# Kernel tuning notes

Hardware: AMD Instinct MI355X
Metric: run time of the kernel (lower is better)

Reference implementation:

```python
import jax, jax.numpy as jnp
import numpy as np

N_NODES = 262144
B_GRAPHS = 1024
NODES_PER_GRAPH = N_NODES // B_GRAPHS
LATENT = 256
HIDDEN = 512
OUT = 3


def setup_inputs() -> dict:
    key = jax.random.key(0)
    ks = jax.random.split(key, 8)
    feat = jax.random.normal(ks[0], (N_NODES, LATENT), dtype=jnp.float32)
    positions = jax.random.normal(ks[1], (N_NODES, 3), dtype=jnp.float32)
    cell = jax.random.normal(ks[2], (B_GRAPHS, 3, 3), dtype=jnp.float32)
    # half of graphs are non-PBC (all-zero cell) -> torque removal applied there
    cell = cell.at[: B_GRAPHS // 2].set(0.0)
    n_node = jnp.full((B_GRAPHS,), NODES_PER_GRAPH, dtype=jnp.int32)
    W0 = jax.random.normal(ks[3], (LATENT, HIDDEN), dtype=jnp.float32) / np.sqrt(LATENT)
    b0 = jnp.zeros((HIDDEN,), dtype=jnp.float32)
    W1 = jax.random.normal(ks[4], (HIDDEN, HIDDEN), dtype=jnp.float32) / np.sqrt(HIDDEN)
    b1 = jnp.zeros((HIDDEN,), dtype=jnp.float32)
    W2 = jax.random.normal(ks[5], (HIDDEN, OUT), dtype=jnp.float32) / np.sqrt(HIDDEN)
    b2 = jnp.zeros((OUT,), dtype=jnp.float32)
    return dict(feat=feat, positions=positions, cell=cell, n_node=n_node,
                W0=W0, b0=b0, W1=W1, b1=b1, W2=W2, b2=b2)


def _mlp(x, W0, b0, W1, b1, W2, b2):
    h = jax.nn.silu(x @ W0 + b0)
    h = jax.nn.silu(h @ W1 + b1)
    return h @ W2 + b2  # [N, 3], raw logits (no output activation)


def _node_head(feat, positions, cell, seg, n_node, W0, b0, W1, b1, W2, b2):
    B = n_node.shape[0]
    counts = n_node.astype(feat.dtype)[:, None]  # [B,1]
    pred = _mlp(feat, W0, b0, W1, b1, W2, b2)  # [N,3]
    # remove per-graph mean
    mean_pred = jax.ops.segment_sum(pred, seg, num_segments=B) / counts
    pred = pred - mean_pred[seg]
    # remove net torque (per-graph analytic Lagrange solution)
    com = jax.ops.segment_sum(positions, seg, num_segments=B) / counts
    r = positions - com[seg]  # com-relative positions [N,3]
    tau = jax.ops.segment_sum(jnp.cross(r, pred), seg, num_segments=B)  # [B,3]
    s = jax.ops.segment_sum(jnp.sum(r * r, axis=1), seg, num_segments=B)  # [B]
    S = jax.ops.segment_sum(r[:, :, None] * r[:, None, :], seg, num_segments=B)  # [B,3,3]
    M = S - s[:, None, None] * jnp.eye(3, dtype=feat.dtype)
    mu = jnp.linalg.solve(M, (-tau)[:, :, None])[:, :, 0]  # [B,3]
    delta = jnp.cross(r, mu[seg])  # [N,3]
    # apply torque removal only to non-PBC graphs (cell all zeros)
    nopbc = jnp.all(cell == 0.0, axis=(1, 2))  # [B]
    return jnp.where(nopbc[seg][:, None], pred + delta, pred)


def reference(feat, positions, cell, n_node, W0, b0, W1, b1, W2, b2):
    N = feat.shape[0]
    B = n_node.shape[0]
    seg = jnp.repeat(jnp.arange(B), n_node, total_repeat_length=N)
    return _node_head(feat, positions, cell, seg, n_node, W0, b0, W1, b1, W2, b2)
```

## Files before the change

### kernel.cpp

```cpp
#include <hip/hip_runtime.h>

#define N_NODES 262144
#define BGRAPHS 1024
#define NPG 256
#define LATENT 256
#define HIDDEN 512
#define BM 128

typedef unsigned short ushort_t;
typedef __attribute__((ext_vector_type(4))) float  f32x4;
typedef __attribute__((ext_vector_type(8))) short  short8;
typedef __attribute__((ext_vector_type(4))) int    int4v;
typedef __attribute__((ext_vector_type(2))) unsigned int uint2v;
typedef __attribute__((ext_vector_type(4))) float  float4v;

__device__ __forceinline__ unsigned int f2bf(float f) {
  union { float f; unsigned int u; } v; v.f = f;
  unsigned int u = v.u;
  return (u + 0x7fffu + ((u >> 16) & 1u)) >> 16;
}
__device__ __forceinline__ unsigned int cvtpk(float lo, float hi) {
  unsigned int r;
  asm("v_cvt_pk_bf16_f32 %0, %1, %2" : "=v"(r) : "v"(lo), "v"(hi));
  return r;
}
__device__ __forceinline__ float silu_f(float x) {
  return x * __builtin_amdgcn_rcpf(1.0f + __expf(-x));
}

__global__ void prep_weights(const float* __restrict__ W0, const float* __restrict__ W1,
                             ushort_t* __restrict__ W0pre, ushort_t* __restrict__ W1pre) {
  int c = blockIdx.x * 256 + threadIdx.x;
  const int C0 = 16384;
  const float* src;
  ushort_t* dst;
  int cc;
  if (c < C0) { src = W0; dst = W0pre; cc = c; }
  else        { src = W1; dst = W1pre; cc = c - C0; }
  int kstep = cc >> 11;
  int p = (cc >> 9) & 3;
  int n = cc & 511;
  int kb = kstep * 32 + p * 8;
  unsigned w[4];
#pragma unroll
  for (int j = 0; j < 4; ++j) {
    unsigned lo = f2bf(src[(size_t)(kb + 2 * j) * HIDDEN + n]);
    unsigned hi = f2bf(src[(size_t)(kb + 2 * j + 1) * HIDDEN + n]);
    w[j] = lo | (hi << 16);
  }
  *(int4v*)(dst + (size_t)cc * 8) = *(int4v*)w;
}

__global__ __launch_bounds__(512) void fused_mlp(
    const float* __restrict__ feat, const ushort_t* __restrict__ W0pre,
    const ushort_t* __restrict__ W1pre, const float* __restrict__ b0,
    const float* __restrict__ b1, const float* __restrict__ W2,
    const float* __restrict__ b2, float* __restrict__ pred) {
  __shared__ __align__(16) char Hc[131072];
  float* Pp = (float*)Hc;

  const int tid = threadIdx.x;
  const int wid = tid >> 6;
  const int lane = tid & 63;
  const int llo = lane & 15;
  const int lhi = lane >> 4;
  const int m0 = blockIdx.x * BM;

  const char* wp = (const char*)W0pre + lhi * 8192 + (wid * 64 + llo) * 16;
  short8 wf0[4], wf1[4];
#pragma unroll
  for (int nt = 0; nt < 4; ++nt) wf0[nt] = *(const short8*)(wp + nt * 256);

  {
    const int m = tid >> 2, q = tid & 3;
    const float* ap = feat + (size_t)(m0 + m) * LATENT + q * 64;
#pragma unroll
    for (int j = 0; j < 2; ++j) {
      const int cch = 2 * q + j;
#pragma unroll
      for (int p = 0; p < 4; ++p) {
        float4v x = *(const float4v*)(ap + j * 32 + p * 8);
        float4v y = *(const float4v*)(ap + j * 32 + p * 8 + 4);
        unsigned u[4];
        u[0] = cvtpk(x[0], x[1]);
        u[1] = cvtpk(x[2], x[3]);
        u[2] = cvtpk(y[0], y[1]);
        u[3] = cvtpk(y[2], y[3]);
        *(int4v*)(Hc + ((cch * 16 + p * 4 + (m >> 5)) << 10) + 512 +
                  (((m & 31) ^ (p << 3)) << 4)) = *(int4v*)u;
      }
    }
  }
  __syncthreads();

  f32x4 acc[4][8];
#pragma unroll
  for (int nt = 0; nt < 4; ++nt)
#pragma unroll
    for (int mt = 0; mt < 8; ++mt) acc[nt][mt] = 0.0f;

  const char* ab = Hc + lhi * 4096 + 512;
  const int xe = ((llo ^ (lhi << 3)) << 4);
  const int xo = (((16 + llo) ^ (lhi << 3)) << 4);

#define MFMA_ALL(WF, XF)                                                                 \
  __builtin_amdgcn_s_setprio(1);                                                         \
  _Pragma("unroll") for (int nt = 0; nt < 4; ++nt)                                       \
  _Pragma("unroll") for (int mt = 0; mt < 8; ++mt)                                       \
      acc[nt][mt] = __builtin_amdgcn_mfma_f32_16x16x32_bf16(WF[nt], XF[mt], acc[nt][mt], \
                                                            0, 0, 0);                    \
  __builtin_amdgcn_s_setprio(0);

#define G1_STEP(SOFF, WA, WB)                                                            \
  {                                                                                      \
    _Pragma("unroll") for (int nt = 0; nt < 4; ++nt)                                     \
        WB[nt] = *(const short8*)(wpp + 32768 + (SOFF) * 32768 + nt * 256);              \
    short8 xf[8];                                                                        \
    _Pragma("unroll") for (int mt = 0; mt < 8; ++mt)                                     \
        xf[mt] = *(const short8*)(abp + (SOFF) * 16384 + ((mt >> 1) << 10) +             \
                                  ((mt & 1) ? xo : xe));                                 \
    MFMA_ALL(WA, xf)                                                                     \
  }

  {
    const char* wpp = wp;
    const char* abp = ab;
#pragma unroll 1
    for (int s = 0; s < 8; s += 2) {
      G1_STEP(0, wf0, wf1)
      G1_STEP(1, wf1, wf0)
      wpp += 65536;
      abp += 32768;
    }
  }

  __syncthreads();
#pragma unroll
  for (int nt = 0; nt < 4; ++nt) {
    int nb = wid * 64 + nt * 16 + lhi * 4;
    float4v bv = *(const float4v*)(b0 + nb);
#pragma unroll
    for (int mt = 0; mt < 8; ++mt) {
      int m = mt * 16 + llo;
      float s0 = silu_f(acc[nt][mt][0] + bv[0]);
      float s1 = silu_f(acc[nt][mt][1] + bv[1]);
      float s2 = silu_f(acc[nt][mt][2] + bv[2]);
      float s3 = silu_f(acc[nt][mt][3] + bv[3]);
      uint2v pk;
      pk.x = cvtpk(s0, s1);
      pk.y = cvtpk(s2, s3);
      *(uint2v*)(Hc + m * 1024 + ((nb * 2) ^ (llo << 4))) = pk;
    }
  }
#pragma unroll
  for (int nt = 0; nt < 4; ++nt)
#pragma unroll
    for (int mt = 0; mt < 8; ++mt) acc[nt][mt] = 0.0f;
  __syncthreads();

#define G2_STEP(T, WA, WB)                                                               \
  {                                                                                      \
    if ((T) < 15) {                                                                      \
      _Pragma("unroll") for (int nt = 0; nt < 4; ++nt)                                   \
          WB[nt] = *(const short8*)(wpp + 32768 + ((T)&1) * 32768 + nt * 256);           \
    }                                                                                    \
    const int col = (((T) * 64 + lhi * 16) ^ (llo << 4));                                \
    short8 xf[8];                                                                        \
    _Pragma("unroll") for (int mt = 0; mt < 8; ++mt)                                     \
        xf[mt] = *(const short8*)(Hc + (mt * 16 + llo) * 1024 + col);                    \
    MFMA_ALL(WA, xf)                                                                     \
  }

  {
    const char* wpp = wp + 8 * 32768;
#pragma unroll 1
    for (int t = 0; t < 16; t += 2) {
      G2_STEP(t, wf0, wf1)
      G2_STEP(t + 1, wf1, wf0)
      wpp += 65536;
    }
  }

  float pacc[8][3];
#pragma unroll
  for (int mt = 0; mt < 8; ++mt) { pacc[mt][0] = 0.f; pacc[mt][1] = 0.f; pacc[mt][2] = 0.f; }
#pragma unroll
  for (int nt = 0; nt < 4; ++nt) {
    int nb = wid * 64 + nt * 16 + lhi * 4;
    float4v bv = *(const float4v*)(b1 + nb);
#pragma unroll
    for (int r = 0; r < 4; ++r) {
      float w20 = W2[(nb + r) * 3 + 0];
      float w21 = W2[(nb + r) * 3 + 1];
      float w22 = W2[(nb + r) * 3 + 2];
#pragma unroll
      for (int mt = 0; mt < 8; ++mt) {
        float h = silu_f(acc[nt][mt][r] + bv[r]);
        pacc[mt][0] += h * w20; pacc[mt][1] += h * w21; pacc[mt][2] += h * w22;
      }
    }
  }
  __syncthreads();
#pragma unroll
  for (int mt = 0; mt < 8; ++mt)
#pragma unroll
    for (int o = 0; o < 3; ++o) {
      float v = pacc[mt][o];
      v += __shfl_xor(v, 16);
      v += __shfl_xor(v, 32);
      if (lane < 16) Pp[wid * 384 + (mt * 16 + llo) * 3 + o] = v;
    }
  __syncthreads();
  if (tid < 384) {
    int m = tid / 3, o = tid - m * 3;
    float v = b2[o];
#pragma unroll
    for (int ww = 0; ww < 8; ++ww) v += Pp[ww * 384 + m * 3 + o];
    pred[(size_t)(m0 + m) * 3 + o] = v;
  }
}

template<int NV>
__device__ __forceinline__ void block_reduce(const float* v, float (*sc)[16], int wid, int lane,
                                             float* tot) {
#pragma unroll
  for (int j = 0; j < NV; ++j) {
    float x = v[j];
#pragma unroll
    for (int off = 32; off >= 1; off >>= 1) x += __shfl_down(x, off);
    if (lane == 0) sc[wid][j] = x;
  }
  __syncthreads();
#pragma unroll
  for (int j = 0; j < NV; ++j) tot[j] = sc[0][j] + sc[1][j] + sc[2][j] + sc[3][j];
  __syncthreads();
}

__global__ __launch_bounds__(256) void finalize_kernel(
    const float* __restrict__ pred, const float* __restrict__ pos,
    const float* __restrict__ cell, const int* __restrict__ n_node,
    float* __restrict__ out) {
  __shared__ float sc[4][16];
  int g = blockIdx.x, tid = threadIdx.x;
  int wid = tid >> 6, lane = tid & 63;
  size_t i = (size_t)g * NPG + tid;

  float p0 = pred[i * 3 + 0], p1 = pred[i * 3 + 1], p2 = pred[i * 3 + 2];
  float q0 = pos[i * 3 + 0], q1 = pos[i * 3 + 1], q2 = pos[i * 3 + 2];

  float v1[6] = {p0, p1, p2, q0, q1, q2};
  float t1[6];
  block_reduce<6>(v1, sc, wid, lane, t1);

  float cnt = (float)n_node[g];
  float pc0 = p0 - t1[0] / cnt, pc1 = p1 - t1[1] / cnt, pc2 = p2 - t1[2] / cnt;
  float r0 = q0 - t1[3] / cnt, r1 = q1 - t1[4] / cnt, r2 = q2 - t1[5] / cnt;

  float v2[10] = {r1 * pc2 - r2 * pc1, r2 * pc0 - r0 * pc2, r0 * pc1 - r1 * pc0,
                  r0 * r0 + r1 * r1 + r2 * r2,
                  r0 * r0, r0 * r1, r0 * r2, r1 * r1, r1 * r2, r2 * r2};
  float t2[10];
  block_reduce<10>(v2, sc, wid, lane, t2);

  double s = (double)t2[3];
  double a = (double)t2[4] - s, b = (double)t2[5], c = (double)t2[6];
  double d = (double)t2[7] - s, e = (double)t2[8], f = (double)t2[9] - s;
  double A00 = d * f - e * e;
  double A01 = c * e - b * f;
  double A02 = b * e - c * d;
  double A11 = a * f - c * c;
  double A12 = b * c - a * e;
  double A22 = a * d - b * b;
  double det = a * A00 + b * A01 + c * A02;
  double rinv = 1.0 / det;
  double rhs0 = -(double)t2[0], rhs1 = -(double)t2[1], rhs2 = -(double)t2[2];
  double mu0 = (A00 * rhs0 + A01 * rhs1 + A02 * rhs2) * rinv;
  double mu1 = (A01 * rhs0 + A11 * rhs1 + A12 * rhs2) * rinv;
  double mu2 = (A02 * rhs0 + A12 * rhs1 + A22 * rhs2) * rinv;

  bool nopbc = true;
#pragma unroll
  for (int j = 0; j < 9; ++j) nopbc = nopbc && (cell[g * 9 + j] == 0.0f);

  float d0 = (float)((double)r1 * mu2 - (double)r2 * mu1);
  float d1 = (float)((double)r2 * mu0 - (double)r0 * mu2);
  float d2 = (float)((double)r0 * mu1 - (double)r1 * mu0);

  out[i * 3 + 0] = pc0 + (nopbc ? d0 : 0.0f);
  out[i * 3 + 1] = pc1 + (nopbc ? d1 : 0.0f);
  out[i * 3 + 2] = pc2 + (nopbc ? d2 : 0.0f);
}

extern "C" void kernel_launch(void* const* d_in, const int* in_sizes, int n_in,
                              void* d_out, int out_size, void* d_ws, size_t ws_size,
                              hipStream_t stream) {
  const float* feat = (const float*)d_in[0];
  const float* positions = (const float*)d_in[1];
  const float* cell = (const float*)d_in[2];
  const int* n_node = (const int*)d_in[3];
  const float* W0 = (const float*)d_in[4];
  const float* b0 = (const float*)d_in[5];
  const float* W1 = (const float*)d_in[6];
  const float* b1 = (const float*)d_in[7];
  const float* W2 = (const float*)d_in[8];
  const float* b2 = (const float*)d_in[9];
  float* out = (float*)d_out;

  char* ws = (char*)d_ws;
  ushort_t* W0pre = (ushort_t*)ws;
  ushort_t* W1pre = (ushort_t*)(ws + 262144);
  float* pred = (float*)(ws + 786432);

  hipLaunchKernelGGL(prep_weights, dim3(192), dim3(256), 0, stream, W0, W1, W0pre, W1pre);
  hipLaunchKernelGGL(fused_mlp, dim3(N_NODES / BM), dim3(512), 0, stream,
                     feat, W0pre, W1pre, b0, b1, W2, b2, pred);
  hipLaunchKernelGGL(finalize_kernel, dim3(BGRAPHS), dim3(256), 0, stream, pred, positions, cell,
                     n_node, out);
}
```

Baseline: 248.5 us.

## Split MLP block into 16 waves with 2x8 warp tiling and fewer accumulators

The fused MLP kernel moves from 8 waves to 16 waves per block. Waves are arranged as 2 row groups by 8 column groups, so each wave holds a 64x64 accumulator tile instead of 128x64. This halves accumulator registers and drops the double-buffered weight fragments in favour of a single buffer refilled after each MFMA batch. The aim is more waves per CU for latency hiding. In exchange, weight fragments are loaded twice as often per block and the weight prefetch no longer overlaps the MFMAs as before.

Result: slower. 420.0 us (+69.0%).

```diff
diff --git a/kernel.cpp b/kernel.cpp
--- a/kernel.cpp
+++ b/kernel.cpp
@@ -51,7 +51,7 @@
   *(int4v*)(dst + (size_t)cc * 8) = *(int4v*)w;
 }
 
-__global__ __launch_bounds__(512) void fused_mlp(
+__global__ __launch_bounds__(1024, 4) void fused_mlp(
     const float* __restrict__ feat, const ushort_t* __restrict__ W0pre,
     const ushort_t* __restrict__ W1pre, const float* __restrict__ b0,
     const float* __restrict__ b1, const float* __restrict__ W2,
@@ -64,84 +64,74 @@
   const int lane = tid & 63;
   const int llo = lane & 15;
   const int lhi = lane >> 4;
+  const int wr = wid & 1;
+  const int wc = wid >> 1;
   const int m0 = blockIdx.x * BM;
 
-  const char* wp = (const char*)W0pre + lhi * 8192 + (wid * 64 + llo) * 16;
-  short8 wf0[4], wf1[4];
-#pragma unroll
-  for (int nt = 0; nt < 4; ++nt) wf0[nt] = *(const short8*)(wp + nt * 256);
+  const char* wp = (const char*)W0pre + lhi * 8192 + (wc * 64 + llo) * 16;
+  short8 wf[4];
+#pragma unroll
+  for (int nt = 0; nt < 4; ++nt) wf[nt] = *(const short8*)(wp + nt * 256);
 
   {
-    const int m = tid >> 2, q = tid & 3;
-    const float* ap = feat + (size_t)(m0 + m) * LATENT + q * 64;
-#pragma unroll
-    for (int j = 0; j < 2; ++j) {
-      const int cch = 2 * q + j;
-#pragma unroll
-      for (int p = 0; p < 4; ++p) {
-        float4v x = *(const float4v*)(ap + j * 32 + p * 8);
-        float4v y = *(const float4v*)(ap + j * 32 + p * 8 + 4);
-        unsigned u[4];
-        u[0] = cvtpk(x[0], x[1]);
-        u[1] = cvtpk(x[2], x[3]);
-        u[2] = cvtpk(y[0], y[1]);
-        u[3] = cvtpk(y[2], y[3]);
-        *(int4v*)(Hc + ((cch * 16 + p * 4 + (m >> 5)) << 10) + 512 +
-                  (((m & 31) ^ (p << 3)) << 4)) = *(int4v*)u;
-      }
-    }
-  }
-  __syncthreads();
-
-  f32x4 acc[4][8];
+    const int m = tid >> 3, cch = tid & 7;
+    const float* ap = feat + (size_t)(m0 + m) * LATENT + cch * 32;
+#pragma unroll
+    for (int p = 0; p < 4; ++p) {
+      float4v x = *(const float4v*)(ap + p * 8);
+      float4v y = *(const float4v*)(ap + p * 8 + 4);
+      unsigned u[4];
+      u[0] = cvtpk(x[0], x[1]);
+      u[1] = cvtpk(x[2], x[3]);
+      u[2] = cvtpk(y[0], y[1]);
+      u[3] = cvtpk(y[2], y[3]);
+      *(int4v*)(Hc + ((cch * 16 + p * 4 + (m >> 5)) << 10) + 512 +
+                (((m & 31) ^ (p << 3)) << 4)) = *(int4v*)u;
+    }
+  }
+  __syncthreads();
+
+  f32x4 acc[4][4];
 #pragma unroll
   for (int nt = 0; nt < 4; ++nt)
 #pragma unroll
-    for (int mt = 0; mt < 8; ++mt) acc[nt][mt] = 0.0f;
-
-  const char* ab = Hc + lhi * 4096 + 512;
-  const int xe = ((llo ^ (lhi << 3)) << 4);
-  const int xo = (((16 + llo) ^ (lhi << 3)) << 4);
-
-#define MFMA_ALL(WF, XF)                                                                 \
+    for (int mt = 0; mt < 4; ++mt) acc[nt][mt] = 0.0f;
+
+#define MFMA_ALL(XF)                                                                     \
   __builtin_amdgcn_s_setprio(1);                                                         \
   _Pragma("unroll") for (int nt = 0; nt < 4; ++nt)                                       \
-  _Pragma("unroll") for (int mt = 0; mt < 8; ++mt)                                       \
-      acc[nt][mt] = __builtin_amdgcn_mfma_f32_16x16x32_bf16(WF[nt], XF[mt], acc[nt][mt], \
+  _Pragma("unroll") for (int mt = 0; mt < 4; ++mt)                                       \
+      acc[nt][mt] = __builtin_amdgcn_mfma_f32_16x16x32_bf16(wf[nt], XF[mt], acc[nt][mt], \
                                                             0, 0, 0);                    \
   __builtin_amdgcn_s_setprio(0);
 
-#define G1_STEP(SOFF, WA, WB)                                                            \
-  {                                                                                      \
-    _Pragma("unroll") for (int nt = 0; nt < 4; ++nt)                                     \
-        WB[nt] = *(const short8*)(wpp + 32768 + (SOFF) * 32768 + nt * 256);              \
-    short8 xf[8];                                                                        \
-    _Pragma("unroll") for (int mt = 0; mt < 8; ++mt)                                     \
-        xf[mt] = *(const short8*)(abp + (SOFF) * 16384 + ((mt >> 1) << 10) +             \
-                                  ((mt & 1) ? xo : xe));                                 \
-    MFMA_ALL(WA, xf)                                                                     \
-  }
-
   {
+    const char* abp = Hc + 512 + (lhi * 4 + wr * 2) * 1024;
+    const int xe = ((llo ^ (lhi << 3)) << 4);
+    const int xo = (((16 + llo) ^ (lhi << 3)) << 4);
     const char* wpp = wp;
-    const char* abp = ab;
 #pragma unroll 1
-    for (int s = 0; s < 8; s += 2) {
-      G1_STEP(0, wf0, wf1)
-      G1_STEP(1, wf1, wf0)
-      wpp += 65536;
-      abp += 32768;
+    for (int s = 0; s < 8; ++s) {
+      short8 xf[4];
+#pragma unroll
+      for (int mt = 0; mt < 4; ++mt)
+        xf[mt] = *(const short8*)(abp + ((mt >> 1) << 10) + ((mt & 1) ? xo : xe));
+      MFMA_ALL(xf)
+#pragma unroll
+      for (int nt = 0; nt < 4; ++nt) wf[nt] = *(const short8*)(wpp + 32768 + nt * 256);
+      wpp += 32768;
+      abp += 16384;
     }
   }
 
   __syncthreads();
 #pragma unroll
   for (int nt = 0; nt < 4; ++nt) {
-    int nb = wid * 64 + nt * 16 + lhi * 4;
+    int nb = wc * 64 + nt * 16 + lhi * 4;
     float4v bv = *(const float4v*)(b0 + nb);
 #pragma unroll
-    for (int mt = 0; mt < 8; ++mt) {
-      int m = mt * 16 + llo;
+    for (int mt = 0; mt < 4; ++mt) {
+      int m = wr * 64 + mt * 16 + llo;
       float s0 = silu_f(acc[nt][mt][0] + bv[0]);
       float s1 = silu_f(acc[nt][mt][1] + bv[1]);
       float s2 = silu_f(acc[nt][mt][2] + bv[2]);
@@ -155,38 +145,34 @@
 #pragma unroll
   for (int nt = 0; nt < 4; ++nt)
 #pragma unroll
-    for (int mt = 0; mt < 8; ++mt) acc[nt][mt] = 0.0f;
-  __syncthreads();
-
-#define G2_STEP(T, WA, WB)                                                               \
-  {                                                                                      \
-    if ((T) < 15) {                                                                      \
-      _Pragma("unroll") for (int nt = 0; nt < 4; ++nt)                                   \
-          WB[nt] = *(const short8*)(wpp + 32768 + ((T)&1) * 32768 + nt * 256);           \
-    }                                                                                    \
-    const int col = (((T) * 64 + lhi * 16) ^ (llo << 4));                                \
-    short8 xf[8];                                                                        \
-    _Pragma("unroll") for (int mt = 0; mt < 8; ++mt)                                     \
-        xf[mt] = *(const short8*)(Hc + (mt * 16 + llo) * 1024 + col);                    \
-    MFMA_ALL(WA, xf)                                                                     \
-  }
+    for (int mt = 0; mt < 4; ++mt) acc[nt][mt] = 0.0f;
+  __syncthreads();
 
   {
+    const char* hrow = Hc + (wr * 64 + llo) * 1024;
     const char* wpp = wp + 8 * 32768;
 #pragma unroll 1
-    for (int t = 0; t < 16; t += 2) {
-      G2_STEP(t, wf0, wf1)
-      G2_STEP(t + 1, wf1, wf0)
-      wpp += 65536;
-    }
-  }
-
-  float pacc[8][3];
-#pragma unroll
-  for (int mt = 0; mt < 8; ++mt) { pacc[mt][0] = 0.f; pacc[mt][1] = 0.f; pacc[mt][2] = 0.f; }
+    for (int t = 0; t < 16; ++t) {
+      const int col = ((t * 64 + lhi * 16) ^ (llo << 4));
+      short8 xf[4];
+#pragma unroll
+      for (int mt = 0; mt < 4; ++mt)
+        xf[mt] = *(const short8*)(hrow + mt * 16384 + col);
+      MFMA_ALL(xf)
+      if (t < 15) {
+#pragma unroll
+        for (int nt = 0; nt < 4; ++nt) wf[nt] = *(const short8*)(wpp + 32768 + nt * 256);
+        wpp += 32768;
+      }
+    }
+  }
+
+  float pacc[4][3];
+#pragma unroll
+  for (int mt = 0; mt < 4; ++mt) { pacc[mt][0] = 0.f; pacc[mt][1] = 0.f; pacc[mt][2] = 0.f; }
 #pragma unroll
   for (int nt = 0; nt < 4; ++nt) {
-    int nb = wid * 64 + nt * 16 + lhi * 4;
+    int nb = wc * 64 + nt * 16 + lhi * 4;
     float4v bv = *(const float4v*)(b1 + nb);
 #pragma unroll
     for (int r = 0; r < 4; ++r) {
@@ -194,7 +180,7 @@
       float w21 = W2[(nb + r) * 3 + 1];
       float w22 = W2[(nb + r) * 3 + 2];
 #pragma unroll
-      for (int mt = 0; mt < 8; ++mt) {
+      for (int mt = 0; mt < 4; ++mt) {
         float h = silu_f(acc[nt][mt][r] + bv[r]);
         pacc[mt][0] += h * w20; pacc[mt][1] += h * w21; pacc[mt][2] += h * w22;
       }
@@ -202,20 +188,21 @@
   }
   __syncthreads();
 #pragma unroll
-  for (int mt = 0; mt < 8; ++mt)
+  for (int mt = 0; mt < 4; ++mt)
 #pragma unroll
     for (int o = 0; o < 3; ++o) {
       float v = pacc[mt][o];
       v += __shfl_xor(v, 16);
       v += __shfl_xor(v, 32);
-      if (lane < 16) Pp[wid * 384 + (mt * 16 + llo) * 3 + o] = v;
+      if (lane < 16) Pp[wid * 192 + (mt * 16 + llo) * 3 + o] = v;
     }
   __syncthreads();
   if (tid < 384) {
     int m = tid / 3, o = tid - m * 3;
+    int wrr = m >> 6, ml = m & 63;
     float v = b2[o];
 #pragma unroll
-    for (int ww = 0; ww < 8; ++ww) v += Pp[ww * 384 + m * 3 + o];
+    for (int ww = 0; ww < 8; ++ww) v += Pp[(2 * ww + wrr) * 192 + ml * 3 + o];
     pred[(size_t)(m0 + m) * 3 + o] = v;
   }
 }
@@ -312,7 +299,7 @@
   float* pred = (float*)(ws + 786432);
 
   hipLaunchKernelGGL(prep_weights, dim3(192), dim3(256), 0, stream, W0, W1, W0pre, W1pre);
-  hipLaunchKernelGGL(fused_mlp, dim3(N_NODES / BM), dim3(512), 0, stream,
+  hipLaunchKernelGGL(fused_mlp, dim3(N_NODES / BM), dim3(1024), 0, stream,
                      feat, W0pre, W1pre, b0, b1, W2, b2, pred);
   hipLaunchKernelGGL(finalize_kernel, dim3(BGRAPHS), dim3(256), 0, stream, pred, positions, cell,
                      n_node, out);
```
